# Performance work log

Measured on AMD Instinct MI355X. Metric: run time of the kernel, lower is better.

The kernel has to match this reference:

```python
import jax, jax.numpy as jnp
import numpy as np

N = 500000
C = 128
G = 4096


def setup_inputs() -> dict:
    key = jax.random.key(0)
    ks = jax.random.split(key, 6)
    x = jax.random.normal(ks[0], (N, C), dtype=jnp.float32)
    proj_w = jax.random.normal(ks[1], (C, C), dtype=jnp.float32) * (1.0 / np.sqrt(C))
    proj_b = jax.random.normal(ks[2], (C,), dtype=jnp.float32) * 0.01
    score_w = jax.random.normal(ks[3], (1, C), dtype=jnp.float32) * (1.0 / np.sqrt(C))
    score_b = jax.random.normal(ks[4], (1,), dtype=jnp.float32) * 0.01
    batch = jnp.sort(jax.random.randint(ks[5], (N,), 0, G, dtype=jnp.int32))
    return {"x": x, "proj_w": proj_w, "proj_b": proj_b,
            "score_w": score_w, "score_b": score_b,
            "batch": batch, "num_graphs": G}


def reference(x, proj_w, proj_b, score_w, score_b, batch, num_graphs):
    # h = tanh(Linear(x)); s = Linear(h) -> [N]
    h = jnp.tanh(x @ proj_w.T + proj_b)
    s = (h @ score_w.T + score_b)[:, 0]  # [N]
    # segment softmax over nodes of each graph
    m = jax.ops.segment_max(s, batch, num_segments=num_graphs)  # [G]
    m = jnp.where(jnp.isfinite(m), m, 0.0)  # guard empty segments
    e = jnp.exp(s - m[batch])
    denom = jax.ops.segment_sum(e, batch, num_segments=num_graphs)  # [G]
    w = e / jnp.maximum(denom[batch], 1e-30)  # [N]
    # weighted scatter-sum of raw features
    pooled = jax.ops.segment_sum(x * w[:, None], batch, num_segments=num_graphs)  # [G, C]
    return pooled
```

## Files before the change

### kernel.cpp

```cpp
#include <hip/hip_runtime.h>
#include <hip/hip_bf16.h>
#include <float.h>
#include <math.h>

#define CDIM 128

typedef __attribute__((ext_vector_type(8))) short short8v;
typedef __attribute__((ext_vector_type(4))) short short4v;
typedef __attribute__((ext_vector_type(4))) float f32x4;

__device__ __forceinline__ short bf16b(float f) {
    __hip_bfloat16 h = __float2bfloat16(f);
    return __builtin_bit_cast(short, h);
}

__device__ __forceinline__ float tanh_fast(float y) {
    float e = __expf(2.0f * y);
    return 1.0f - 2.0f / (e + 1.0f);
}

__device__ __forceinline__ int lower_bound_i(const int* __restrict__ b, int n, int v) {
    int lo = 0, hi = n;
    while (lo < hi) { int mid = (lo + hi) >> 1; if (b[mid] < v) lo = mid + 1; else hi = mid; }
    return lo;
}

__global__ void seg_bounds_kernel(const int* __restrict__ batch, int N, int G,
                                  int* __restrict__ seg) {
    int g = blockIdx.x * blockDim.x + threadIdx.x;
    if (g < G) seg[g] = lower_bound_i(batch, N, g);
    if (g == 0) seg[G] = N;
}

__global__ void wconv_kernel(const float* __restrict__ proj_w, short* __restrict__ wfrag) {
    int tid = blockIdx.x * 256 + threadIdx.x;
    int f = tid >> 6, l = tid & 63;
    int c  = ((f >> 2) << 4) | (l & 15);
    int k0 = ((f & 3) << 5) | ((l >> 4) << 3);
    short8v v;
    #pragma unroll
    for (int j = 0; j < 8; ++j) v[j] = bf16b(proj_w[c * CDIM + k0 + j]);
    ((short8v*)wfrag)[tid] = v;
}

__launch_bounds__(256, 3)
__global__ void pool_kernel(const float* __restrict__ x,
                            const short* __restrict__ wfrag,
                            const float* __restrict__ proj_b,
                            const float* __restrict__ score_w,
                            const float* __restrict__ score_b,
                            const int* __restrict__ seg,
                            float* __restrict__ out,
                            int N) {
    __shared__ short XsB[64 * 128];
    __shared__ float ps[4 * 64];
    __shared__ float cs[64];
    __shared__ __align__(16) float red[8 * 128];
    __shared__ float bc[2];

    const int g = blockIdx.x;
    const int t = threadIdx.x;
    const int lane = t & 63;
    const int w = t >> 6;
    const int start = seg[g];
    const int cnt = seg[g + 1] - start;

    if (cnt <= 0) {
        if (t < CDIM) out[g * CDIM + t] = 0.0f;
        return;
    }

    const float4* __restrict__ x4 = (const float4*)x;
    const int g8 = t >> 5;
    const int c4 = t & 31;
    const int al = lane & 15, ah = lane >> 4;

    float4 xr[8], xn[8];
    #pragma unroll
    for (int i = 0; i < 8; ++i) {
        int row = g8 + (i << 3);
        size_t gr = (size_t)min(start + row, N - 1);
        xr[i] = x4[gr * 32 + c4];
    }

    short8v wf[2][4];
    {
        const short8v* wfg = (const short8v*)wfrag;
        #pragma unroll
        for (int j = 0; j < 2; ++j)
            #pragma unroll
            for (int ks = 0; ks < 4; ++ks)
                wf[j][ks] = wfg[((((w << 1) | j) << 2 | ks) << 6) | lane];
    }
    float swl[2], pbl[2];
    #pragma unroll
    for (int j = 0; j < 2; ++j) {
        swl[j] = score_w[(((w << 1) | j) << 4) + al];
        pbl[j] = proj_b[(((w << 1) | j) << 4) + al];
    }
    const float sb = score_b[0];

    float m_run = -FLT_MAX, l_run = 0.0f;
    float4 pa = make_float4(0.f, 0.f, 0.f, 0.f);

    for (int cb = 0; cb < cnt; cb += 64) {
        const int chunk_n = min(64, cnt - cb);

        #pragma unroll
        for (int i = 0; i < 8; ++i) {
            int row = g8 + (i << 3);
            short4v b;
            b[0] = bf16b(xr[i].x); b[1] = bf16b(xr[i].y);
            b[2] = bf16b(xr[i].z); b[3] = bf16b(xr[i].w);
            *(short4v*)&XsB[(row << 7) | ((c4 << 2) ^ ((row & 7) << 3))] = b;
        }
        __syncthreads();

        const bool pf = (cb + 64 < cnt);
        if (pf) {
            #pragma unroll
            for (int i = 0; i < 8; ++i) {
                int row = g8 + (i << 3);
                size_t gr = (size_t)min(start + cb + 64 + row, N - 1);
                xn[i] = x4[gr * 32 + c4];
            }
        }

        #pragma unroll
        for (int rt = 0; rt < 4; ++rt) {
            const int arow = (rt << 4) | al;
            const int rsw = (arow & 7) << 3;
            f32x4 a0 = (f32x4){0.f, 0.f, 0.f, 0.f};
            f32x4 a1 = (f32x4){0.f, 0.f, 0.f, 0.f};
            #pragma unroll
            for (int ks = 0; ks < 4; ++ks) {
                short8v af = *(const short8v*)&XsB[(arow << 7) | (((ks << 5) | (ah << 3)) ^ rsw)];
                a0 = __builtin_amdgcn_mfma_f32_16x16x32_bf16(af, wf[0][ks], a0, 0, 0, 0);
                a1 = __builtin_amdgcn_mfma_f32_16x16x32_bf16(af, wf[1][ks], a1, 0, 0, 0);
            }
            #pragma unroll
            for (int r = 0; r < 4; ++r) {
                float s = swl[0] * tanh_fast(a0[r] + pbl[0])
                        + swl[1] * tanh_fast(a1[r] + pbl[1]);
                s += __shfl_xor(s, 1); s += __shfl_xor(s, 2);
                s += __shfl_xor(s, 4); s += __shfl_xor(s, 8);
                if (al == 0) ps[(w << 6) | (rt << 4) | (ah << 2) | r] = s;
            }
        }
        __syncthreads();

        if (t < 64) {
            float v = (t < chunk_n)
                    ? (ps[t] + ps[64 + t] + ps[128 + t] + ps[192 + t] + sb)
                    : -FLT_MAX;
            float mx = v;
            mx = fmaxf(mx, __shfl_xor(mx, 1));  mx = fmaxf(mx, __shfl_xor(mx, 2));
            mx = fmaxf(mx, __shfl_xor(mx, 4));  mx = fmaxf(mx, __shfl_xor(mx, 8));
            mx = fmaxf(mx, __shfl_xor(mx, 16)); mx = fmaxf(mx, __shfl_xor(mx, 32));
            float m_new = fmaxf(m_run, mx);
            float sc = __expf(m_run - m_new);
            float e = (t < chunk_n) ? __expf(v - m_new) : 0.f;
            float ssum = e;
            ssum += __shfl_xor(ssum, 1);  ssum += __shfl_xor(ssum, 2);
            ssum += __shfl_xor(ssum, 4);  ssum += __shfl_xor(ssum, 8);
            ssum += __shfl_xor(ssum, 16); ssum += __shfl_xor(ssum, 32);
            cs[t] = e;
            if (t == 0) { bc[0] = sc; bc[1] = ssum; }
            m_run = m_new;
        }
        __syncthreads();

        const float sc = bc[0];
        l_run = l_run * sc + bc[1];
        pa.x *= sc; pa.y *= sc; pa.z *= sc; pa.w *= sc;
        #pragma unroll
        for (int i = 0; i < 8; ++i) {
            float e = cs[g8 + (i << 3)];
            pa.x += e * xr[i].x; pa.y += e * xr[i].y;
            pa.z += e * xr[i].z; pa.w += e * xr[i].w;
        }

        if (pf) {
            #pragma unroll
            for (int i = 0; i < 8; ++i) xr[i] = xn[i];
        }
    }

    *(float4*)&red[(g8 << 7) + (c4 << 2)] = pa;
    __syncthreads();
    if (t < CDIM) {
        float v = 0.f;
        #pragma unroll
        for (int j = 0; j < 8; ++j) v += red[j * CDIM + t];
        out[g * CDIM + t] = v * (1.0f / fmaxf(l_run, 1e-30f));
    }
}

extern "C" void kernel_launch(void* const* d_in, const int* in_sizes, int n_in,
                              void* d_out, int out_size, void* d_ws, size_t ws_size,
                              hipStream_t stream) {
    const float* x       = (const float*)d_in[0];
    const float* proj_w  = (const float*)d_in[1];
    const float* proj_b  = (const float*)d_in[2];
    const float* score_w = (const float*)d_in[3];
    const float* score_b = (const float*)d_in[4];
    const int*   batch   = (const int*)d_in[5];

    const int N = in_sizes[0] / CDIM;
    const int G = out_size / CDIM;

    int*   seg   = (int*)d_ws;
    short* wfrag = (short*)((char*)d_ws + (((size_t)(G + 1) * 4 + 255) & ~(size_t)255));

    seg_bounds_kernel<<<(G + 255) / 256, 256, 0, stream>>>(batch, N, G, seg);
    wconv_kernel<<<8, 256, 0, stream>>>(proj_w, wfrag);
    pool_kernel<<<G, 256, 0, stream>>>(x, wfrag, proj_b, score_w, score_b,
                                       seg, (float*)d_out, N);
}
```

Baseline: 108.3 us.

## Double-buffer fp32 x tiles in LDS and compute softmax redundantly per wave

The x chunk is now staged in LDS as fp32 in a swizzled double buffer instead of being converted to bf16 at store time. The bf16 conversion moves to MFMA operand load, and the weighted accumulation reads x back from LDS rather than from registers. Every wave now repeats the online-softmax max/sum itself and broadcasts weights with shuffles, which drops one barrier and the cs/bc shared arrays per chunk. The costs are larger LDS use (64KB), launch bounds lowered to 2 blocks per SM, and more conversion work per MFMA tile.

Measured after the change: 248.7 us. 2.3x slower.

```diff
diff --git a/kernel.cpp b/kernel.cpp
--- a/kernel.cpp
+++ b/kernel.cpp
@@ -6,7 +6,6 @@
 #define CDIM 128
 
 typedef __attribute__((ext_vector_type(8))) short short8v;
-typedef __attribute__((ext_vector_type(4))) short short4v;
 typedef __attribute__((ext_vector_type(4))) float f32x4;
 
 __device__ __forceinline__ short bf16b(float f) {
@@ -43,7 +42,11 @@
     ((short8v*)wfrag)[tid] = v;
 }
 
-__launch_bounds__(256, 3)
+__device__ __forceinline__ int swz_slot(int row, int c4) {
+    return (row << 5) | ((((c4 >> 1) ^ (row & 7)) << 1) | (c4 & 1));
+}
+
+__launch_bounds__(256, 2)
 __global__ void pool_kernel(const float* __restrict__ x,
                             const short* __restrict__ wfrag,
                             const float* __restrict__ proj_b,
@@ -52,11 +55,8 @@
                             const int* __restrict__ seg,
                             float* __restrict__ out,
                             int N) {
-    __shared__ short XsB[64 * 128];
-    __shared__ float ps[4 * 64];
-    __shared__ float cs[64];
-    __shared__ __align__(16) float red[8 * 128];
-    __shared__ float bc[2];
+    __shared__ float4 Xf[2][64 * 32];
+    __shared__ float  ps[64 * 4];
 
     const int g = blockIdx.x;
     const int t = threadIdx.x;
@@ -64,23 +64,27 @@
     const int w = t >> 6;
     const int start = seg[g];
     const int cnt = seg[g + 1] - start;
+    float4* og4 = (float4*)(out + (size_t)g * CDIM);
 
     if (cnt <= 0) {
-        if (t < CDIM) out[g * CDIM + t] = 0.0f;
+        if (t < 32) og4[t] = make_float4(0.f, 0.f, 0.f, 0.f);
         return;
     }
 
     const float4* __restrict__ x4 = (const float4*)x;
-    const int g8 = t >> 5;
     const int c4 = t & 31;
-    const int al = lane & 15, ah = lane >> 4;
-
-    float4 xr[8], xn[8];
-    #pragma unroll
-    for (int i = 0; i < 8; ++i) {
-        int row = g8 + (i << 3);
-        size_t gr = (size_t)min(start + row, N - 1);
-        xr[i] = x4[gr * 32 + c4];
+    const int rp = t >> 5;
+    const int rl = lane & 15, kq = lane >> 4;
+
+    float4 xn[8];
+    {
+        const int rem0 = cnt;
+        #pragma unroll
+        for (int i = 0; i < 8; ++i) {
+            int row = (i << 3) | rp;
+            size_t gr = (size_t)(start + min(row, rem0 - 1));
+            xn[i] = x4[gr * 32 + c4];
+        }
     }
 
     short8v wf[2][4];
@@ -95,48 +99,54 @@
     float swl[2], pbl[2];
     #pragma unroll
     for (int j = 0; j < 2; ++j) {
-        swl[j] = score_w[(((w << 1) | j) << 4) + al];
-        pbl[j] = proj_b[(((w << 1) | j) << 4) + al];
+        swl[j] = score_w[(((w << 1) | j) << 4) + rl];
+        pbl[j] = proj_b[(((w << 1) | j) << 4) + rl];
     }
     const float sb = score_b[0];
+
+    #pragma unroll
+    for (int i = 0; i < 8; ++i)
+        Xf[0][swz_slot((i << 3) | rp, c4)] = xn[i];
+    int buf = 0;
 
     float m_run = -FLT_MAX, l_run = 0.0f;
     float4 pa = make_float4(0.f, 0.f, 0.f, 0.f);
 
     for (int cb = 0; cb < cnt; cb += 64) {
-        const int chunk_n = min(64, cnt - cb);
-
-        #pragma unroll
-        for (int i = 0; i < 8; ++i) {
-            int row = g8 + (i << 3);
-            short4v b;
-            b[0] = bf16b(xr[i].x); b[1] = bf16b(xr[i].y);
-            b[2] = bf16b(xr[i].z); b[3] = bf16b(xr[i].w);
-            *(short4v*)&XsB[(row << 7) | ((c4 << 2) ^ ((row & 7) << 3))] = b;
-        }
+        const int rem = cnt - cb;
         __syncthreads();
 
         const bool pf = (cb + 64 < cnt);
         if (pf) {
+            const int rem2 = cnt - cb - 64;
             #pragma unroll
             for (int i = 0; i < 8; ++i) {
-                int row = g8 + (i << 3);
-                size_t gr = (size_t)min(start + cb + 64 + row, N - 1);
+                int row = (i << 3) | rp;
+                size_t gr = (size_t)(start + cb + 64 + min(row, rem2 - 1));
                 xn[i] = x4[gr * 32 + c4];
             }
         }
 
+        const float4* Xc = Xf[buf];
         #pragma unroll
         for (int rt = 0; rt < 4; ++rt) {
-            const int arow = (rt << 4) | al;
-            const int rsw = (arow & 7) << 3;
+            const int arow = (rt << 4) | rl;
+            short8v af[4];
+            #pragma unroll
+            for (int ks = 0; ks < 4; ++ks) {
+                int q = (arow << 5) | ((((ks << 2) | kq) ^ (arow & 7)) << 1);
+                float4 q0 = Xc[q], q1 = Xc[q + 1];
+                af[ks][0] = bf16b(q0.x); af[ks][1] = bf16b(q0.y);
+                af[ks][2] = bf16b(q0.z); af[ks][3] = bf16b(q0.w);
+                af[ks][4] = bf16b(q1.x); af[ks][5] = bf16b(q1.y);
+                af[ks][6] = bf16b(q1.z); af[ks][7] = bf16b(q1.w);
+            }
             f32x4 a0 = (f32x4){0.f, 0.f, 0.f, 0.f};
             f32x4 a1 = (f32x4){0.f, 0.f, 0.f, 0.f};
             #pragma unroll
             for (int ks = 0; ks < 4; ++ks) {
-                short8v af = *(const short8v*)&XsB[(arow << 7) | (((ks << 5) | (ah << 3)) ^ rsw)];
-                a0 = __builtin_amdgcn_mfma_f32_16x16x32_bf16(af, wf[0][ks], a0, 0, 0, 0);
-                a1 = __builtin_amdgcn_mfma_f32_16x16x32_bf16(af, wf[1][ks], a1, 0, 0, 0);
+                a0 = __builtin_amdgcn_mfma_f32_16x16x32_bf16(af[ks], wf[0][ks], a0, 0, 0, 0);
+                a1 = __builtin_amdgcn_mfma_f32_16x16x32_bf16(af[ks], wf[1][ks], a1, 0, 0, 0);
             }
             #pragma unroll
             for (int r = 0; r < 4; ++r) {
@@ -144,55 +154,58 @@
                         + swl[1] * tanh_fast(a1[r] + pbl[1]);
                 s += __shfl_xor(s, 1); s += __shfl_xor(s, 2);
                 s += __shfl_xor(s, 4); s += __shfl_xor(s, 8);
-                if (al == 0) ps[(w << 6) | (rt << 4) | (ah << 2) | r] = s;
+                if (rl == 0) ps[(((rt << 4) | (kq << 2) | r) << 2) | w] = s;
             }
         }
         __syncthreads();
 
-        if (t < 64) {
-            float v = (t < chunk_n)
-                    ? (ps[t] + ps[64 + t] + ps[128 + t] + ps[192 + t] + sb)
-                    : -FLT_MAX;
-            float mx = v;
-            mx = fmaxf(mx, __shfl_xor(mx, 1));  mx = fmaxf(mx, __shfl_xor(mx, 2));
-            mx = fmaxf(mx, __shfl_xor(mx, 4));  mx = fmaxf(mx, __shfl_xor(mx, 8));
-            mx = fmaxf(mx, __shfl_xor(mx, 16)); mx = fmaxf(mx, __shfl_xor(mx, 32));
-            float m_new = fmaxf(m_run, mx);
-            float sc = __expf(m_run - m_new);
-            float e = (t < chunk_n) ? __expf(v - m_new) : 0.f;
-            float ssum = e;
-            ssum += __shfl_xor(ssum, 1);  ssum += __shfl_xor(ssum, 2);
-            ssum += __shfl_xor(ssum, 4);  ssum += __shfl_xor(ssum, 8);
-            ssum += __shfl_xor(ssum, 16); ssum += __shfl_xor(ssum, 32);
-            cs[t] = e;
-            if (t == 0) { bc[0] = sc; bc[1] = ssum; }
-            m_run = m_new;
-        }
-        __syncthreads();
-
-        const float sc = bc[0];
-        l_run = l_run * sc + bc[1];
+        float4 pp = *(const float4*)&ps[lane << 2];
+        float sv = (lane < rem) ? (pp.x + pp.y + pp.z + pp.w + sb) : -FLT_MAX;
+        float mx = sv;
+        #pragma unroll
+        for (int m = 1; m < 64; m <<= 1) mx = fmaxf(mx, __shfl_xor(mx, m));
+        const float m_new = fmaxf(m_run, mx);
+        float ev = (lane < rem) ? __expf(sv - m_new) : 0.f;
+        float ssum = ev;
+        #pragma unroll
+        for (int m = 1; m < 64; m <<= 1) ssum += __shfl_xor(ssum, m);
+        const float sc = __expf(m_run - m_new);
+        m_run = m_new;
+        l_run = l_run * sc + ssum;
         pa.x *= sc; pa.y *= sc; pa.z *= sc; pa.w *= sc;
+
         #pragma unroll
         for (int i = 0; i < 8; ++i) {
-            float e = cs[g8 + (i << 3)];
-            pa.x += e * xr[i].x; pa.y += e * xr[i].y;
-            pa.z += e * xr[i].z; pa.w += e * xr[i].w;
+            int row = (i << 3) | rp;
+            float em = __shfl(ev, row);
+            float4 xv = Xc[swz_slot(row, c4)];
+            pa.x += em * xv.x; pa.y += em * xv.y;
+            pa.z += em * xv.z; pa.w += em * xv.w;
         }
 
         if (pf) {
-            #pragma unroll
-            for (int i = 0; i < 8; ++i) xr[i] = xn[i];
-        }
-    }
-
-    *(float4*)&red[(g8 << 7) + (c4 << 2)] = pa;
+            float4* Xn = Xf[buf ^ 1];
+            #pragma unroll
+            for (int i = 0; i < 8; ++i)
+                Xn[swz_slot((i << 3) | rp, c4)] = xn[i];
+        }
+        buf ^= 1;
+    }
+
     __syncthreads();
-    if (t < CDIM) {
-        float v = 0.f;
-        #pragma unroll
-        for (int j = 0; j < 8; ++j) v += red[j * CDIM + t];
-        out[g * CDIM + t] = v * (1.0f / fmaxf(l_run, 1e-30f));
+    float4* red = Xf[0];
+    red[(rp << 5) | c4] = pa;
+    __syncthreads();
+    if (t < 32) {
+        float4 v = make_float4(0.f, 0.f, 0.f, 0.f);
+        #pragma unroll
+        for (int j = 0; j < 8; ++j) {
+            float4 r = red[(j << 5) | t];
+            v.x += r.x; v.y += r.y; v.z += r.z; v.w += r.w;
+        }
+        const float inv = 1.0f / fmaxf(l_run, 1e-30f);
+        v.x *= inv; v.y *= inv; v.z *= inv; v.w *= inv;
+        og4[t] = v;
     }
 }
 
```
